# Kernel tuning notes

Measured on AMD Instinct MI355X. Metric: run time of the kernel, lower is better.

Reference implementation:

```python
import jax, jax.numpy as jnp
from jax import lax
import numpy as np

IN_DIM = 38
T = 300
H1 = 32
H2 = 20
FC1 = 80  # 2 timesteps * (H2 fw + H2 bw)
FC2 = 20
FC3 = 3


def _lstm_scan(x, W, b, h_dim):
    """BasicLSTMCell (forget_bias=1.0) over time. x: [B,T,D] -> [B,T,h_dim]."""
    B = x.shape[0]

    def step(carry, xt):
        c, h = carry
        z = jnp.concatenate([xt, h], axis=-1) @ W + b  # [B, 4h]
        i, j, f, o = jnp.split(z, 4, axis=-1)          # TF gate order: i, j, f, o
        c = c * jax.nn.sigmoid(f + 1.0) + jax.nn.sigmoid(i) * jnp.tanh(j)
        h = jnp.tanh(c) * jax.nn.sigmoid(o)
        return (c, h), h

    init = (jnp.zeros((B, h_dim), x.dtype), jnp.zeros((B, h_dim), x.dtype))
    _, hs = lax.scan(step, init, jnp.swapaxes(x, 0, 1))  # [T,B,h]
    return jnp.swapaxes(hs, 0, 1)


def _stack2(x, W1, b1, W2, b2):
    h1 = _lstm_scan(x, W1, b1, H1)
    return _lstm_scan(h1, W2, b2, H2)


def setup_inputs() -> dict:
    key = jax.random.key(0)
    ks = jax.random.split(key, 16)
    s = 0.1
    d = {
        "x": jax.random.normal(ks[0], (2048, T, IN_DIM), jnp.float32),
        # forward-direction stacked LSTM
        "Wf1": jax.random.normal(ks[1], (IN_DIM + H1, 4 * H1), jnp.float32) * s,
        "bf1": jnp.zeros((4 * H1,), jnp.float32),
        "Wf2": jax.random.normal(ks[2], (H1 + H2, 4 * H2), jnp.float32) * s,
        "bf2": jnp.zeros((4 * H2,), jnp.float32),
        # backward-direction stacked LSTM
        "Wb1": jax.random.normal(ks[3], (IN_DIM + H1, 4 * H1), jnp.float32) * s,
        "bb1": jnp.zeros((4 * H1,), jnp.float32),
        "Wb2": jax.random.normal(ks[4], (H1 + H2, 4 * H2), jnp.float32) * s,
        "bb2": jnp.zeros((4 * H2,), jnp.float32),
        # FC head
        "W_fc1": jax.random.normal(ks[5], (FC1, FC1), jnp.float32) * s,
        "b_fc1": jnp.zeros((FC1,), jnp.float32),
        "W_fc2": jax.random.normal(ks[6], (FC1, FC2), jnp.float32) * s,
        "b_fc2": jnp.zeros((FC2,), jnp.float32),
        "W_fc3": jax.random.normal(ks[7], (FC2, FC3), jnp.float32) * s,
        "b_fc3": jnp.zeros((FC3,), jnp.float32),
    }
    return d


def reference(x, Wf1, bf1, Wf2, bf2, Wb1, bb1, Wb2, bb2,
              W_fc1, b_fc1, W_fc2, b_fc2, W_fc3, b_fc3):
    # forward direction
    fw = _stack2(x, Wf1, bf1, Wf2, bf2)                     # [B,T,H2]
    # backward direction: reverse time, scan, reverse back
    bw = _stack2(x[:, ::-1], Wb1, bb1, Wb2, bb2)[:, ::-1]   # [B,T,H2]
    rnn_out = jnp.concatenate([fw, bw], axis=-1)            # [B,T,2*H2]
    # concat first and last timestep -> [B, 80] (== reshape of [B,2,40])
    feat = jnp.concatenate([rnn_out[:, 0], rnn_out[:, -1]], axis=-1)
    h = jnp.tanh(feat @ W_fc1 + b_fc1)
    h = jnp.tanh(h @ W_fc2 + b_fc2)
    logits = h @ W_fc3 + b_fc3                              # [B,3]
    return logits.reshape(-1, 3, 1)
```

## Files before the change

### kernel.cpp

```cpp
#include <hip/hip_runtime.h>
#include <hip/hip_bf16.h>

#define TSTEPS 300
#define INDIM  38
#define NB     8

typedef __attribute__((ext_vector_type(4))) float    float4_;
typedef __attribute__((ext_vector_type(2))) float    float2_;
typedef __attribute__((ext_vector_type(8))) short    short8;
typedef unsigned short ushort_;

__device__ __forceinline__ float frcp(float x){ return __builtin_amdgcn_rcpf(x); }
__device__ __forceinline__ float fexp2(float x){ float r; asm("v_exp_f32 %0, %1" : "=v"(r) : "v"(x)); return r; }
__device__ __forceinline__ float fsig(float x){ return frcp(1.0f + fexp2(-1.44269504f*x)); }
__device__ __forceinline__ float ftanh(float x){ return 1.0f - 2.0f*frcp(1.0f + fexp2(2.88539008f*x)); }
__device__ __forceinline__ unsigned bf16rne(float f){
    unsigned u = __float_as_uint(f);
    return (u + 0x7FFFu + ((u>>16)&1u)) >> 16;
}
__device__ __forceinline__ int posk(int rel){ return 8*((rel&15)>>2) + (rel&3) + 4*(rel>>4); }
__device__ __forceinline__ short8 ldf(const ushort_* p){ return *(const short8*)p; }
__device__ __forceinline__ float4_ bmfma(short8 a, short8 b, float4_ c){
    return __builtin_amdgcn_mfma_f32_16x16x32_bf16(a, b, c, 0, 0, 0);
}
#define BAR() do{ asm volatile("s_waitcnt lgkmcnt(0)" ::: "memory"); \
                  __builtin_amdgcn_s_barrier(); \
                  asm volatile("" ::: "memory"); }while(0)

__global__ __launch_bounds__(256,2) void rnn_kernel(
    const float* __restrict__ x,
    const float* __restrict__ Wf1, const float* __restrict__ bf1,
    const float* __restrict__ Wf2, const float* __restrict__ bf2,
    const float* __restrict__ Wb1, const float* __restrict__ bb1,
    const float* __restrict__ Wb2, const float* __restrict__ bb2,
    float* __restrict__ featws)
{
    __shared__ __attribute__((aligned(16))) ushort_ W1Fl[8][16][104];
    __shared__ __attribute__((aligned(16))) ushort_ W2Fl[5][16][72];
    __shared__ __attribute__((aligned(16))) ushort_ inHh[2][16][40],  inHl[2][16][40];
    __shared__ __attribute__((aligned(16))) ushort_ inXh[2][16][104], inXl[2][16][104];
    __shared__ __attribute__((aligned(16))) ushort_ h2Ah[2][16][40],  h2Al[2][16][40];
    __shared__ float z2s[8][84];

    const int tid = threadIdx.x;
    const int dir = blockIdx.y;
    const int b0  = blockIdx.x * NB;

    const float* W1s = dir ? Wb1 : Wf1;
    const float* b1s = dir ? bb1 : bf1;
    const float* W2s = dir ? Wb2 : Wf2;
    const float* b2s = dir ? bb2 : bf2;

    for (int i = tid; i < 8*16*104; i += 256) ((ushort_*)W1Fl)[i] = 0;
    for (int i = tid; i < 5*16*72;  i += 256) ((ushort_*)W2Fl)[i] = 0;
    for (int i = tid; i < 2*16*40;  i += 256){ ((ushort_*)inHh)[i]=0; ((ushort_*)inHl)[i]=0;
                                               ((ushort_*)h2Ah)[i]=0; ((ushort_*)h2Al)[i]=0; }
    for (int i = tid; i < 2*16*104; i += 256){ ((ushort_*)inXh)[i]=0; ((ushort_*)inXl)[i]=0; }
    __syncthreads();
    for (int idx = tid; idx < 70*128; idx += 256){
        int k = idx >> 7, c = idx & 127;
        int kp = (k < INDIM) ? (k + 32) : (k - INDIM);
        float w = W1s[idx];
        unsigned hu = bf16rne(w);
        W1Fl[c>>4][c&15][(kp>>5)*32 + posk(kp&31)] =
            (ushort_)bf16rne(w - __uint_as_float(hu<<16));
    }
    for (int idx = tid; idx < 52*80; idx += 256){
        int k = idx / 80, c = idx % 80;
        float w = W2s[idx];
        unsigned hu = bf16rne(w);
        W2Fl[c/16][c&15][(k>>5)*32 + posk(k&31)] =
            (ushort_)bf16rne(w - __uint_as_float(hu<<16));
    }
    for (int idx = tid; idx < NB*INDIM; idx += 256){
        int t0 = dir ? (TSTEPS-1) : 0;
        int b = idx / INDIM, k = idx % INDIM;
        int off = (k>>5)*32 + posk(k&31);
        float w = x[((size_t)(b0+b)*TSTEPS + t0)*INDIM + k];
        unsigned hu = bf16rne(w);
        inXh[0][b][off] = (ushort_)hu;
        inXl[0][b][off] = (ushort_)bf16rne(w - __uint_as_float(hu<<16));
    }

    const int wv = tid >> 6;
    const int ln = tid & 63;
    const int g  = ln >> 4;
    const int cl = ln & 15;
    const int g8 = 8*g;
    const int dstep = dir ? -INDIM : INDIM;

    short8 B1h[4][3];
    float bq[4] = {0,0,0,0};
    int pc1 = 0;
    float c1[4] = {0.f,0.f,0.f,0.f};
    short8 B2h[5][2];
    float bz2[5] = {0,0,0,0,0};
    bool zmask = false;
    bool c2v[2] = {false,false}; int c2r[2]={0,0}, c2c[2]={0,0}, c2p[2]={0,0};
    float c2st[2] = {0.f,0.f};
    bool stv[2] = {false,false}; int stb[2]={0,0}, stoff[2]={0,0};
    const float* stp[2] = {x,x}; float2_ xr[2] = {{0,0},{0,0}};

    if (wv < 2){
        #pragma unroll
        for (int q = 0; q < 4; ++q){
            const int t = wv + 2*q;
            #pragma unroll
            for (int kt = 0; kt < 3; ++kt){
                union { short8 s; ushort_ u[8]; } H;
                #pragma unroll
                for (int j = 0; j < 8; ++j){
                    int kp = kt*32 + ((j<4) ? (4*g+j) : (16+4*g+j-4));
                    float w = 0.f;
                    if (kp < 70){
                        int row = (kp < 32) ? (38+kp) : (kp-32);
                        w = W1s[row*128 + 16*t + cl];
                    }
                    H.u[j] = (ushort_)bf16rne(w);
                }
                B1h[q][kt] = H.s;
            }
        }
        const int c = 16*wv + cl;
        pc1 = posk(c);
        bq[0] = b1s[c]; bq[1] = b1s[c+32]; bq[2] = b1s[c+64] + 1.0f; bq[3] = b1s[c+96];
    } else {
        #pragma unroll
        for (int t = 0; t < 5; ++t){
            #pragma unroll
            for (int kt = 0; kt < 2; ++kt){
                union { short8 s; ushort_ u[8]; } H;
                #pragma unroll
                for (int j = 0; j < 8; ++j){
                    int kp = kt*32 + ((j<4) ? (4*g+j) : (16+4*g+j-4));
                    float w = 0.f;
                    if (kp < 52) w = W2s[kp*80 + 16*t + cl];
                    H.u[j] = (ushort_)bf16rne(w);
                }
                B2h[t][kt] = H.s;
            }
            int col = 16*t + cl;
            bz2[t] = b2s[col] + ((col/20)==2 ? 1.f : 0.f);
        }
        zmask = (wv==2) ? (g==0) : (g==1);
        #pragma unroll
        for (int m = 0; m < 2; ++m){
            int e = ln + 64*m; c2v[m] = (e < 80);
            int es = c2v[m] ? e : 0;
            c2r[m] = 4*(wv-2) + es/20; c2c[m] = es%20; c2p[m] = posk(es%20);
        }
        const int sid = (wv-2)*64 + ln;
        int t1 = dir ? (TSTEPS-2) : 1;
        #pragma unroll
        for (int m = 0; m < 2; ++m){
            int e = sid + 128*m; stv[m] = (e < NB*19);
            int es = stv[m] ? e : 0;
            int b = es / 19, k = 2*(es % 19);
            stb[m] = b; stoff[m] = (k>>5)*32 + posk(k&31);
            stp[m] = x + ((size_t)(b0+b)*TSTEPS + t1)*INDIM + k;
            if (stv[m]){ xr[m] = *(const float2_*)stp[m]; stp[m] += dstep; }
        }
    }
    __syncthreads();

    auto phase = [&](int p, int PX){
        const int PR = PX ^ 1;
        if (wv < 2){
            if (p < TSTEPS){
                short8 Ah[3], Al[3];
                Ah[0] = ldf(&inHh[PR][cl][g8]);      Al[0] = ldf(&inHl[PR][cl][g8]);
                Ah[1] = ldf(&inXh[PX][cl][g8]);      Al[1] = ldf(&inXl[PX][cl][g8]);
                Ah[2] = ldf(&inXh[PX][cl][32+g8]);   Al[2] = ldf(&inXl[PX][cl][32+g8]);
                float4_ hh[4], hl[4], lh[4];
                #pragma unroll
                for (int q = 0; q < 4; ++q){
                    hh[q] = float4_{bq[q],bq[q],bq[q],bq[q]};
                    hl[q] = float4_{0,0,0,0};
                    lh[q] = float4_{0,0,0,0};
                }
                #pragma unroll
                for (int kt = 0; kt < 3; ++kt){
                    #pragma unroll
                    for (int q = 0; q < 4; ++q) hh[q] = bmfma(Ah[kt], B1h[q][kt], hh[q]);
                }
                #pragma unroll
                for (int kt = 0; kt < 3; ++kt){
                    #pragma unroll
                    for (int q = 0; q < 4; ++q){
                        short8 bl = ldf(&W1Fl[wv + 2*q][cl][kt*32 + g8]);
                        hl[q] = bmfma(Ah[kt], bl, hl[q]);
                    }
                }
                #pragma unroll
                for (int kt = 0; kt < 3; ++kt){
                    #pragma unroll
                    for (int q = 0; q < 4; ++q) lh[q] = bmfma(Al[kt], B1h[q][kt], lh[q]);
                }
                float4_ a0 = hh[0]+hl[0]+lh[0];
                float4_ a1 = hh[1]+hl[1]+lh[1];
                float4_ a2 = hh[2]+hl[2]+lh[2];
                float4_ a3 = hh[3]+hl[3]+lh[3];
                #pragma unroll
                for (int r = 0; r < 4; ++r){
                    float si = fsig(a0[r]);
                    float tj = ftanh(a1[r]);
                    float sf = fsig(a2[r]);
                    float so = fsig(a3[r]);
                    c1[r] = fmaf(c1[r], sf, si*tj);
                    float h = ftanh(c1[r]) * so;
                    unsigned hu = bf16rne(h);
                    inHh[PX][4*g+r][pc1] = (ushort_)hu;
                    inHl[PX][4*g+r][pc1] = (ushort_)bf16rne(h - __uint_as_float(hu<<16));
                }
            }
        } else {
            if (p <= TSTEPS-2){
                #pragma unroll
                for (int m = 0; m < 2; ++m) if (stv[m]){
                    unsigned h0 = bf16rne(xr[m].x);
                    unsigned l0 = bf16rne(xr[m].x - __uint_as_float(h0<<16));
                    unsigned h1v = bf16rne(xr[m].y);
                    unsigned l1v = bf16rne(xr[m].y - __uint_as_float(h1v<<16));
                    *(unsigned*)&inXh[PR][stb[m]][stoff[m]] = h0 | (h1v<<16);
                    *(unsigned*)&inXl[PR][stb[m]][stoff[m]] = l0 | (l1v<<16);
                }
            }
            if (p <= TSTEPS-3){
                #pragma unroll
                for (int m = 0; m < 2; ++m) if (stv[m]){ xr[m] = *(const float2_*)stp[m]; stp[m] += dstep; }
            }
            if (p >= 1){
                short8 Ah0 = ldf(&inHh[PR][cl][g8]), Al0 = ldf(&inHl[PR][cl][g8]);
                short8 Gh  = ldf(&h2Ah[PR][cl][g8]), Gl  = ldf(&h2Al[PR][cl][g8]);
                float4_ hh[5], hl[5], lh[5];
                #pragma unroll
                for (int t = 0; t < 5; ++t){
                    hh[t] = float4_{bz2[t],bz2[t],bz2[t],bz2[t]};
                    hl[t] = float4_{0,0,0,0};
                    lh[t] = float4_{0,0,0,0};
                }
                #pragma unroll
                for (int t = 0; t < 5; ++t) hh[t] = bmfma(Ah0, B2h[t][0], hh[t]);
                #pragma unroll
                for (int t = 0; t < 5; ++t) hh[t] = bmfma(Gh,  B2h[t][1], hh[t]);
                #pragma unroll
                for (int t = 0; t < 5; ++t){
                    short8 bl0 = ldf(&W2Fl[t][cl][g8]);
                    hl[t] = bmfma(Ah0, bl0, hl[t]);
                }
                #pragma unroll
                for (int t = 0; t < 5; ++t){
                    short8 bl1 = ldf(&W2Fl[t][cl][32 + g8]);
                    hl[t] = bmfma(Gh, bl1, hl[t]);
                }
                #pragma unroll
                for (int t = 0; t < 5; ++t) lh[t] = bmfma(Al0, B2h[t][0], lh[t]);
                #pragma unroll
                for (int t = 0; t < 5; ++t) lh[t] = bmfma(Gl,  B2h[t][1], lh[t]);
                if (zmask){
                    #pragma unroll
                    for (int t = 0; t < 5; ++t){
                        float4_ a = hh[t] + hl[t] + lh[t];
                        #pragma unroll
                        for (int r = 0; r < 4; ++r) z2s[4*g + r][16*t + cl] = a[r];
                    }
                }
                #pragma unroll
                for (int m = 0; m < 2; ++m) if (c2v[m]){
                    const int rw = c2r[m], c = c2c[m];
                    float zi = z2s[rw][c],    zj = z2s[rw][c+20];
                    float zf = z2s[rw][c+40], zo = z2s[rw][c+60];
                    c2st[m] = fmaf(c2st[m], fsig(zf), fsig(zi)*ftanh(zj));
                    float h = ftanh(c2st[m]) * fsig(zo);
                    unsigned hu = bf16rne(h);
                    h2Ah[PX][rw][c2p[m]] = (ushort_)hu;
                    h2Al[PX][rw][c2p[m]] = (ushort_)bf16rne(h - __uint_as_float(hu<<16));
                    if (p == 1 || p == TSTEPS){
                        int off = (p == 1) ? (dir ? 60 : 0) : (dir ? 20 : 40);
                        featws[(size_t)(b0+rw)*80 + off + c] = h;
                    }
                }
            }
        }
        BAR();
    };

    for (int pp = 0; pp < TSTEPS; pp += 2){
        phase(pp, 0);
        phase(pp+1, 1);
    }
    phase(TSTEPS, 0);
}

__global__ __launch_bounds__(64) void fc_kernel(
    const float* __restrict__ featws,
    const float* __restrict__ Wfc1, const float* __restrict__ bfc1,
    const float* __restrict__ Wfc2, const float* __restrict__ bfc2,
    const float* __restrict__ Wfc3, const float* __restrict__ bfc3,
    float* __restrict__ out)
{
    __shared__ float f[80];
    __shared__ float h1b[80];
    __shared__ float h2b[20];
    const int b = blockIdx.x;
    const int lane = threadIdx.x;

    for (int i = lane; i < 80; i += 64) f[i] = featws[(size_t)b*80 + i];
    __syncthreads();
    for (int j = lane; j < 80; j += 64){
        float s = bfc1[j];
        #pragma unroll 8
        for (int k = 0; k < 80; ++k) s += f[k]*Wfc1[k*80 + j];
        h1b[j] = ftanh(s);
    }
    __syncthreads();
    if (lane < 20){
        float s = bfc2[lane];
        #pragma unroll 8
        for (int k = 0; k < 80; ++k) s += h1b[k]*Wfc2[k*20 + lane];
        h2b[lane] = ftanh(s);
    }
    __syncthreads();
    if (lane < 3){
        float s = bfc3[lane];
        #pragma unroll
        for (int k = 0; k < 20; ++k) s += h2b[k]*Wfc3[k*3 + lane];
        out[(size_t)b*3 + lane] = s;
    }
}

extern "C" void kernel_launch(void* const* d_in, const int* in_sizes, int n_in,
                              void* d_out, int out_size, void* d_ws, size_t ws_size,
                              hipStream_t stream) {
    const float* x    = (const float*)d_in[0];
    const float* Wf1  = (const float*)d_in[1];
    const float* bf1  = (const float*)d_in[2];
    const float* Wf2  = (const float*)d_in[3];
    const float* bf2  = (const float*)d_in[4];
    const float* Wb1  = (const float*)d_in[5];
    const float* bb1  = (const float*)d_in[6];
    const float* Wb2  = (const float*)d_in[7];
    const float* bb2  = (const float*)d_in[8];
    const float* Wfc1 = (const float*)d_in[9];
    const float* bfc1 = (const float*)d_in[10];
    const float* Wfc2 = (const float*)d_in[11];
    const float* bfc2 = (const float*)d_in[12];
    const float* Wfc3 = (const float*)d_in[13];
    const float* bfc3 = (const float*)d_in[14];

    float* feat = (float*)d_ws;

    rnn_kernel<<<dim3(2048/NB, 2), 256, 0, stream>>>(
        x, Wf1, bf1, Wf2, bf2, Wb1, bb1, Wb2, bb2, feat);
    fc_kernel<<<2048, 64, 0, stream>>>(
        feat, Wfc1, bfc1, Wfc2, bfc2, Wfc3, bfc3, (float*)d_out);
}
```

Baseline: 389.1 us.

## Halve layer-1 gate math via lane shuffles, merge MFMA accumulators, use hardware bf16 cvt

The layer-1 gate activations only need rows 0-7, since NB=8. Before, each lane evaluated all 4 accumulator rows. Now the upper half-wave swaps in rows 2-3 with __shfl_xor, so each lane evaluates 2 rows and the transcendental work on the serial recurrence path roughly halves. The hi*hi and hi*lo MFMA chains now share one accumulator, which drops an add stage and some registers. Software bf16 rounding is replaced with v_cvt_pk_bf16_f32, which adds the risk of small numeric differences and of dependent MFMA chains with longer latency.

```diff
diff --git a/kernel.cpp b/kernel.cpp
--- a/kernel.cpp
+++ b/kernel.cpp
@@ -17,6 +17,12 @@
 __device__ __forceinline__ unsigned bf16rne(float f){
     unsigned u = __float_as_uint(f);
     return (u + 0x7FFFu + ((u>>16)&1u)) >> 16;
+}
+__device__ __forceinline__ unsigned cvt1(float f){
+    unsigned r; asm("v_cvt_pk_bf16_f32 %0,%1,%1" : "=v"(r) : "v"(f)); return r;
+}
+__device__ __forceinline__ unsigned cvt2(float a, float b){
+    unsigned r; asm("v_cvt_pk_bf16_f32 %0,%1,%2" : "=v"(r) : "v"(a), "v"(b)); return r;
 }
 __device__ __forceinline__ int posk(int rel){ return 8*((rel&15)>>2) + (rel&3) + 4*(rel>>4); }
 __device__ __forceinline__ short8 ldf(const ushort_* p){ return *(const short8*)p; }
@@ -91,8 +97,8 @@
 
     short8 B1h[4][3];
     float bq[4] = {0,0,0,0};
-    int pc1 = 0;
-    float c1[4] = {0.f,0.f,0.f,0.f};
+    int pc1 = 0, r1row0 = 0, r1row1 = 0;
+    float c1a = 0.f, c1b = 0.f;
     short8 B2h[5][2];
     float bz2[5] = {0,0,0,0,0};
     bool zmask = false;
@@ -124,6 +130,8 @@
         const int c = 16*wv + cl;
         pc1 = posk(c);
         bq[0] = b1s[c]; bq[1] = b1s[c+32]; bq[2] = b1s[c+64] + 1.0f; bq[3] = b1s[c+96];
+        r1row0 = 4*(g&1) + ((ln >= 32) ? 2 : 0);
+        r1row1 = r1row0 + 1;
     } else {
         #pragma unroll
         for (int t = 0; t < 5; ++t){
@@ -171,24 +179,23 @@
                 Ah[0] = ldf(&inHh[PR][cl][g8]);      Al[0] = ldf(&inHl[PR][cl][g8]);
                 Ah[1] = ldf(&inXh[PX][cl][g8]);      Al[1] = ldf(&inXl[PX][cl][g8]);
                 Ah[2] = ldf(&inXh[PX][cl][32+g8]);   Al[2] = ldf(&inXl[PX][cl][32+g8]);
-                float4_ hh[4], hl[4], lh[4];
+                float4_ ac[4], lh[4];
                 #pragma unroll
                 for (int q = 0; q < 4; ++q){
-                    hh[q] = float4_{bq[q],bq[q],bq[q],bq[q]};
-                    hl[q] = float4_{0,0,0,0};
+                    ac[q] = float4_{bq[q],bq[q],bq[q],bq[q]};
                     lh[q] = float4_{0,0,0,0};
                 }
                 #pragma unroll
                 for (int kt = 0; kt < 3; ++kt){
                     #pragma unroll
-                    for (int q = 0; q < 4; ++q) hh[q] = bmfma(Ah[kt], B1h[q][kt], hh[q]);
+                    for (int q = 0; q < 4; ++q) ac[q] = bmfma(Ah[kt], B1h[q][kt], ac[q]);
                 }
                 #pragma unroll
                 for (int kt = 0; kt < 3; ++kt){
                     #pragma unroll
                     for (int q = 0; q < 4; ++q){
                         short8 bl = ldf(&W1Fl[wv + 2*q][cl][kt*32 + g8]);
-                        hl[q] = bmfma(Ah[kt], bl, hl[q]);
+                        ac[q] = bmfma(Ah[kt], bl, ac[q]);
                     }
                 }
                 #pragma unroll
@@ -196,33 +203,35 @@
                     #pragma unroll
                     for (int q = 0; q < 4; ++q) lh[q] = bmfma(Al[kt], B1h[q][kt], lh[q]);
                 }
-                float4_ a0 = hh[0]+hl[0]+lh[0];
-                float4_ a1 = hh[1]+hl[1]+lh[1];
-                float4_ a2 = hh[2]+hl[2]+lh[2];
-                float4_ a3 = hh[3]+hl[3]+lh[3];
-                #pragma unroll
-                for (int r = 0; r < 4; ++r){
-                    float si = fsig(a0[r]);
-                    float tj = ftanh(a1[r]);
-                    float sf = fsig(a2[r]);
-                    float so = fsig(a3[r]);
-                    c1[r] = fmaf(c1[r], sf, si*tj);
-                    float h = ftanh(c1[r]) * so;
-                    unsigned hu = bf16rne(h);
-                    inHh[PX][4*g+r][pc1] = (ushort_)hu;
-                    inHl[PX][4*g+r][pc1] = (ushort_)bf16rne(h - __uint_as_float(hu<<16));
-                }
+                float4_ a0 = ac[0]+lh[0], a1 = ac[1]+lh[1];
+                float4_ a2 = ac[2]+lh[2], a3 = ac[3]+lh[3];
+                float s02=__shfl_xor(a0[2],32), s12=__shfl_xor(a1[2],32),
+                      s22=__shfl_xor(a2[2],32), s32=__shfl_xor(a3[2],32);
+                float s03=__shfl_xor(a0[3],32), s13=__shfl_xor(a1[3],32),
+                      s23=__shfl_xor(a2[3],32), s33=__shfl_xor(a3[3],32);
+                const bool up = (ln >= 32);
+                float zi0 = up?s02:a0[0], zj0 = up?s12:a1[0], zf0 = up?s22:a2[0], zo0 = up?s32:a3[0];
+                float zi1 = up?s03:a0[1], zj1 = up?s13:a1[1], zf1 = up?s23:a2[1], zo1 = up?s33:a3[1];
+                c1a = fmaf(c1a, fsig(zf0), fsig(zi0)*ftanh(zj0));
+                float h0 = ftanh(c1a) * fsig(zo0);
+                c1b = fmaf(c1b, fsig(zf1), fsig(zi1)*ftanh(zj1));
+                float h1 = ftanh(c1b) * fsig(zo1);
+                unsigned p0 = cvt1(h0);
+                inHh[PX][r1row0][pc1] = (ushort_)p0;
+                inHl[PX][r1row0][pc1] = (ushort_)cvt1(h0 - __uint_as_float(p0<<16));
+                unsigned p1 = cvt1(h1);
+                inHh[PX][r1row1][pc1] = (ushort_)p1;
+                inHl[PX][r1row1][pc1] = (ushort_)cvt1(h1 - __uint_as_float(p1<<16));
             }
         } else {
             if (p <= TSTEPS-2){
                 #pragma unroll
                 for (int m = 0; m < 2; ++m) if (stv[m]){
-                    unsigned h0 = bf16rne(xr[m].x);
-                    unsigned l0 = bf16rne(xr[m].x - __uint_as_float(h0<<16));
-                    unsigned h1v = bf16rne(xr[m].y);
-                    unsigned l1v = bf16rne(xr[m].y - __uint_as_float(h1v<<16));
-                    *(unsigned*)&inXh[PR][stb[m]][stoff[m]] = h0 | (h1v<<16);
-                    *(unsigned*)&inXl[PR][stb[m]][stoff[m]] = l0 | (l1v<<16);
+                    unsigned hp = cvt2(xr[m].x, xr[m].y);
+                    *(unsigned*)&inXh[PR][stb[m]][stoff[m]] = hp;
+                    float l0 = xr[m].x - __uint_as_float(hp<<16);
+                    float l1 = xr[m].y - __uint_as_float(hp & 0xFFFF0000u);
+                    *(unsigned*)&inXl[PR][stb[m]][stoff[m]] = cvt2(l0, l1);
                 }
             }
             if (p <= TSTEPS-3){
@@ -232,26 +241,25 @@
             if (p >= 1){
                 short8 Ah0 = ldf(&inHh[PR][cl][g8]), Al0 = ldf(&inHl[PR][cl][g8]);
                 short8 Gh  = ldf(&h2Ah[PR][cl][g8]), Gl  = ldf(&h2Al[PR][cl][g8]);
-                float4_ hh[5], hl[5], lh[5];
+                float4_ ac[5], lh[5];
                 #pragma unroll
                 for (int t = 0; t < 5; ++t){
-                    hh[t] = float4_{bz2[t],bz2[t],bz2[t],bz2[t]};
-                    hl[t] = float4_{0,0,0,0};
+                    ac[t] = float4_{bz2[t],bz2[t],bz2[t],bz2[t]};
                     lh[t] = float4_{0,0,0,0};
                 }
                 #pragma unroll
-                for (int t = 0; t < 5; ++t) hh[t] = bmfma(Ah0, B2h[t][0], hh[t]);
-                #pragma unroll
-                for (int t = 0; t < 5; ++t) hh[t] = bmfma(Gh,  B2h[t][1], hh[t]);
+                for (int t = 0; t < 5; ++t) ac[t] = bmfma(Ah0, B2h[t][0], ac[t]);
+                #pragma unroll
+                for (int t = 0; t < 5; ++t) ac[t] = bmfma(Gh,  B2h[t][1], ac[t]);
                 #pragma unroll
                 for (int t = 0; t < 5; ++t){
                     short8 bl0 = ldf(&W2Fl[t][cl][g8]);
-                    hl[t] = bmfma(Ah0, bl0, hl[t]);
+                    ac[t] = bmfma(Ah0, bl0, ac[t]);
                 }
                 #pragma unroll
                 for (int t = 0; t < 5; ++t){
                     short8 bl1 = ldf(&W2Fl[t][cl][32 + g8]);
-                    hl[t] = bmfma(Gh, bl1, hl[t]);
+                    ac[t] = bmfma(Gh, bl1, ac[t]);
                 }
                 #pragma unroll
                 for (int t = 0; t < 5; ++t) lh[t] = bmfma(Al0, B2h[t][0], lh[t]);
@@ -260,7 +268,7 @@
                 if (zmask){
                     #pragma unroll
                     for (int t = 0; t < 5; ++t){
-                        float4_ a = hh[t] + hl[t] + lh[t];
+                        float4_ a = ac[t] + lh[t];
                         #pragma unroll
                         for (int r = 0; r < 4; ++r) z2s[4*g + r][16*t + cl] = a[r];
                     }
@@ -272,9 +280,9 @@
                     float zf = z2s[rw][c+40], zo = z2s[rw][c+60];
                     c2st[m] = fmaf(c2st[m], fsig(zf), fsig(zi)*ftanh(zj));
                     float h = ftanh(c2st[m]) * fsig(zo);
-                    unsigned hu = bf16rne(h);
-                    h2Ah[PX][rw][c2p[m]] = (ushort_)hu;
-                    h2Al[PX][rw][c2p[m]] = (ushort_)bf16rne(h - __uint_as_float(hu<<16));
+                    unsigned hp = cvt1(h);
+                    h2Ah[PX][rw][c2p[m]] = (ushort_)hp;
+                    h2Al[PX][rw][c2p[m]] = (ushort_)cvt1(h - __uint_as_float(hp<<16));
                     if (p == 1 || p == TSTEPS){
                         int off = (p == 1) ? (dir ? 60 : 0) : (dir ? 20 : 40);
                         featws[(size_t)(b0+rw)*80 + off + c] = h;
```

Result: faster. 349.5 us (-10.2%).
